# Kernel tuning notes

Measured on AMD Instinct MI355X. Metric: run time of the kernel, lower is better.

## Reference

```python
import jax, jax.numpy as jnp
import numpy as np

B, T, D, NH, FF, L, NCLS, CELL = 4, 64, 128, 4, 512, 2, 7, 64
DIMS = (600, 342, 300)


def layernorm(x, g, b, eps=1e-5):
    m = jnp.mean(x, -1, keepdims=True)
    v = jnp.mean((x - m) ** 2, -1, keepdims=True)
    return (x - m) / jnp.sqrt(v + eps) * g + b


def mha(x, Wqkv, bqkv, Wo, bo):
    N, S, Dm = x.shape
    hd = Dm // NH
    q, k, v = jnp.split(x @ Wqkv + bqkv, 3, axis=-1)
    q = q.reshape(N, S, NH, hd).transpose(0, 2, 1, 3) / jnp.float32(hd) ** 0.5
    k = k.reshape(N, S, NH, hd).transpose(0, 2, 1, 3)
    v = v.reshape(N, S, NH, hd).transpose(0, 2, 1, 3)
    att = jax.nn.softmax(jnp.einsum('nhqd,nhkd->nhqk', q, k), axis=-1)
    o = jnp.einsum('nhqk,nhkd->nhqd', att, v).transpose(0, 2, 1, 3).reshape(N, S, Dm)
    return o @ Wo + bo


def _l2norm(x):
    return x / jnp.maximum(jnp.linalg.norm(x, axis=-1, keepdims=True), 1e-12)


def _model(x_text, x_vis, x_aud, Wp_text, bp_text, Wp_vis, bp_vis, Wp_aud, bp_aud,
           lang1, lang2, Wl1, bl1, Wl2, bl2, phase_text, phase_vis, phase_aud,
           t_Wqkv, t_bqkv, t_Wo, t_bo, t_g1, t_b1, t_W1, t_bf1, t_W2, t_bf2, t_g2, t_b2,
           meas_r, meas_i, fc_W1, fc_b1, fc_W2, fc_b2):
    b, t = x_text.shape[0], x_text.shape[1]
    # modality projections + ReLU
    reps = [jax.nn.relu(x @ W + bb) for x, W, bb in
            ((x_text, Wp_text, bp_text), (x_vis, Wp_vis, bp_vis), (x_aud, Wp_aud, bp_aud))]
    l1 = jnp.broadcast_to(lang1, (b, t, lang1.shape[-1]))
    l2 = jnp.broadcast_to(lang2, (b, t, lang2.shape[-1]))
    lrep1 = jax.nn.relu(l1 @ Wl1 + bl1)
    lrep2 = jax.nn.relu(l2 @ Wl2 + bl2)
    amps = [_l2norm(r) for r in reps]
    lamp1, lamp2 = _l2norm(lrep1), _l2norm(lrep2)
    # phase embedding: smask is all-ones so index is always 0 -> single learned phase vector
    phases = [jnp.broadcast_to(p, (b, t, D)) for p in (phase_text, phase_vis, phase_aud)]
    cmul = lambda ph, a: (a * jnp.cos(ph), a * jnp.sin(ph))
    pure = [cmul(ph, a) for ph, a in zip(phases, amps)]
    ls1 = cmul(phases[0], lamp1)
    ls2 = cmul(phases[0], lamp2)
    # Hadamard gate analog on (real, imag)
    s2 = jnp.float32(2.0) ** -0.5
    h1 = ((ls1[0] + ls1[1]) * s2, (ls1[0] - ls1[1]) * s2)
    h2 = ((ls2[0] + ls2[1]) * s2, (ls2[0] - ls2[1]) * s2)
    # CNOT-style entanglement: complex elementwise product, renormalized to a pure state
    er = h1[0] * h2[0] - h1[1] * h2[1]
    ei = h1[0] * h2[1] + h1[1] * h2[0]
    en = jnp.maximum(jnp.sqrt(jnp.sum(er * er + ei * ei, -1, keepdims=True)), 1e-12)
    ent = (er / en, ei / en)

    def outer(st):  # rho = v v^dagger, v = r + i*im
        r, i = st
        rr = jnp.einsum('btd,bte->btde', r, r) + jnp.einsum('btd,bte->btde', i, i)
        ri = jnp.einsum('btd,bte->btde', i, r) - jnp.einsum('btd,bte->btde', r, i)
        return rr, ri

    mats = [outer(s) for s in pure] + [outer(ent)]
    w = jnp.concatenate([jnp.linalg.norm(r, axis=-1, keepdims=True)
                         for r in reps + [lrep1]], -1)
    w = jax.nn.softmax(w, -1)  # [B,T,4]
    rho_r = sum(w[..., m:m + 1, None] * mats[m][0] for m in range(4))
    rho_i = sum(w[..., m:m + 1, None] * mats[m][1] for m in range(4))
    # seq blocks: same block applied independently per timestep to real and imag parts
    # -> vectorize the Python loop over T (and the real/imag pair) into one batch dim
    x = jnp.concatenate([rho_r, rho_i], 0).reshape(2 * b * t, D, D)
    for l in range(L):
        x = layernorm(x + mha(x, t_Wqkv[l], t_bqkv[l], t_Wo[l], t_bo[l]), t_g1[l], t_b1[l])
        x = layernorm(x + (jax.nn.relu(x @ t_W1[l] + t_bf1[l]) @ t_W2[l] + t_bf2[l]),
                      t_g2[l], t_b2[l])
    x = x.reshape(2, b, t, D, D)
    rho_r, rho_i = x[0], x[1]
    # quantum measurement: p_k = Re(v_k^dagger rho v_k), v_k normalized complex vectors
    mn = jnp.maximum(jnp.sqrt(jnp.sum(meas_r ** 2 + meas_i ** 2, -1, keepdims=True)), 1e-12)
    vr, vi = meas_r / mn, meas_i / mn  # [K=D, D]
    ar = jnp.einsum('btde,ke->btkd', rho_r, vr) - jnp.einsum('btde,ke->btkd', rho_i, vi)
    ai = jnp.einsum('btde,ke->btkd', rho_r, vi) + jnp.einsum('btde,ke->btkd', rho_i, vr)
    probs = jnp.einsum('kd,btkd->btk', vr, ar) + jnp.einsum('kd,btkd->btk', vi, ai)
    logits = jax.nn.relu(probs @ fc_W1 + fc_b1) @ fc_W2 + fc_b2
    return jax.nn.log_softmax(logits, -1)  # [B,T,NCLS]


def setup_inputs():
    key = jax.random.key(0)
    ks = iter(jax.random.split(key, 32))
    rn = lambda shape, s=0.05: jax.random.normal(next(ks), shape, dtype=jnp.float32) * s
    z = lambda shape: jnp.zeros(shape, jnp.float32)
    o = lambda shape: jnp.ones(shape, jnp.float32)
    return dict(
        x_text=rn((B, T, DIMS[0]), 1.0), x_vis=rn((B, T, DIMS[1]), 1.0), x_aud=rn((B, T, DIMS[2]), 1.0),
        Wp_text=rn((DIMS[0], D)), bp_text=z((D,)),
        Wp_vis=rn((DIMS[1], D)), bp_vis=z((D,)),
        Wp_aud=rn((DIMS[2], D)), bp_aud=z((D,)),
        lang1=rn((1, 1, DIMS[2]), 1.0), lang2=rn((1, 1, DIMS[2]), 1.0),
        Wl1=rn((DIMS[2], D)), bl1=z((D,)), Wl2=rn((DIMS[2], D)), bl2=z((D,)),
        phase_text=rn((D,), 1.0), phase_vis=rn((D,), 1.0), phase_aud=rn((D,), 1.0),
        t_Wqkv=rn((L, D, 3 * D)), t_bqkv=z((L, 3 * D)),
        t_Wo=rn((L, D, D)), t_bo=z((L, D)),
        t_g1=o((L, D)), t_b1=z((L, D)),
        t_W1=rn((L, D, FF)), t_bf1=z((L, FF)),
        t_W2=rn((L, FF, D)), t_bf2=z((L, D)),
        t_g2=o((L, D)), t_b2=z((L, D)),
        meas_r=rn((D, D), 1.0), meas_i=rn((D, D), 1.0),
        fc_W1=rn((D, CELL)), fc_b1=z((CELL,)), fc_W2=rn((CELL, NCLS)), fc_b2=z((NCLS,)),
    )


def reference(x_text, x_vis, x_aud, Wp_text, bp_text, Wp_vis, bp_vis, Wp_aud, bp_aud,
              lang1, lang2, Wl1, bl1, Wl2, bl2, phase_text, phase_vis, phase_aud,
              t_Wqkv, t_bqkv, t_Wo, t_bo, t_g1, t_b1, t_W1, t_bf1, t_W2, t_bf2, t_g2, t_b2,
              meas_r, meas_i, fc_W1, fc_b1, fc_W2, fc_b2):
    return _model(x_text, x_vis, x_aud, Wp_text, bp_text, Wp_vis, bp_vis, Wp_aud, bp_aud,
                  lang1, lang2, Wl1, bl1, Wl2, bl2, phase_text, phase_vis, phase_aud,
                  t_Wqkv, t_bqkv, t_Wo, t_bo, t_g1, t_b1, t_W1, t_bf1, t_W2, t_bf2, t_g2, t_b2,
                  meas_r, meas_i, fc_W1, fc_b1, fc_W2, fc_b2)
```

## Files before the change

kernel.cpp:

```cpp
#include <hip/hip_runtime.h>
#include <hip/hip_bf16.h>

typedef __hip_bfloat16 bf16;
typedef short short8 __attribute__((ext_vector_type(8)));
typedef float f32x4 __attribute__((ext_vector_type(4)));

__device__ __forceinline__ float b2f(bf16 v){ return __bfloat162float(v); }

__device__ __forceinline__ short f2bs(float f){
  union { __hip_bfloat16 b; short s; } u; u.b = __float2bfloat16(f); return u.s;
}
__device__ __forceinline__ float bs2f(short s){
  union { short s; __hip_bfloat16 b; } u; u.s = s; return __bfloat162float(u.b);
}

__device__ __forceinline__ float wred_sum(float v){
  #pragma unroll
  for (int o = 32; o > 0; o >>= 1) v += __shfl_xor(v, o, 64);
  return v;
}

__device__ __forceinline__ void gload_lds16(const void* g, void* l){
  __builtin_amdgcn_global_load_lds((const __attribute__((address_space(1))) unsigned*)g,
                                   (__attribute__((address_space(3))) unsigned*)l, 16, 0, 0);
}

__device__ __forceinline__ unsigned swzA(unsigned a){ return a ^ (((a >> 8) & 7u) << 4); }
__device__ __forceinline__ unsigned swzB(unsigned a){ return a ^ (((a >> 7) & 3u) << 4); }

template<int DIMN>
__device__ void modality(const float* x, const float* W, const float* bia, const float* ph,
                         float* PURE, float* RNORM, int m, int bt, float* xs, float* red)
{
  int tid = threadIdx.x;
  for (int i = tid; i < DIMN; i += 128) xs[i] = x[bt*DIMN + i];
  __syncthreads();
  float a0 = 0.f, a1 = 0.f, a2 = 0.f, a3 = 0.f;
  int k = 0;
  for (; k + 4 <= DIMN; k += 4){
    a0 = fmaf(xs[k],   W[(k  )*128 + tid], a0);
    a1 = fmaf(xs[k+1], W[(k+1)*128 + tid], a1);
    a2 = fmaf(xs[k+2], W[(k+2)*128 + tid], a2);
    a3 = fmaf(xs[k+3], W[(k+3)*128 + tid], a3);
  }
  for (; k < DIMN; k++) a0 = fmaf(xs[k], W[k*128 + tid], a0);
  float acc = bia[tid] + ((a0 + a1) + (a2 + a3));
  float rep = fmaxf(acc, 0.f);
  float s = wred_sum(rep*rep);
  int wid = tid >> 6, lane = tid & 63;
  if (lane == 0) red[wid] = s;
  __syncthreads();
  float nrm = sqrtf(red[0] + red[1]);
  float amp = rep / fmaxf(nrm, 1e-12f);
  float p = ph[tid];
  PURE[bt*768 + m*128 + tid]       = amp * cosf(p);
  PURE[bt*768 + (3+m)*128 + tid]   = amp * sinf(p);
  if (tid == 0) RNORM[bt*4 + m] = nrm;
}

__global__ void prep_kernel(
    const float* __restrict__ Wqkv, const float* __restrict__ Wo,
    const float* __restrict__ W1, const float* __restrict__ W2,
    short* __restrict__ WqkvT, short* __restrict__ WoT,
    short* __restrict__ W1T, short* __restrict__ W2T,
    const float* xt, const float* xv, const float* xa,
    const float* Wpt, const float* bpt, const float* Wpv, const float* bpv,
    const float* Wpa, const float* bpa,
    const float* pht, const float* phv, const float* pha,
    float* PURE, float* RNORM,
    const float* l1, const float* l2,
    const float* Wl1, const float* bl1, const float* Wl2, const float* bl2,
    float* LANGB,
    const float* mr, const float* mi, float* VMEAS, short* VMEASB)
{
  __shared__ float xs[600];
  __shared__ float xs2a[300];
  __shared__ float red[4];
  int b = blockIdx.x, tid = threadIdx.x;

  if (b < 384){
    int l = b / 192, bb = b - l*192;
    const float* in; short* out; int K, N, boff;
    bool isW2 = false;
    if (bb < 48)      { in = Wqkv; out = WqkvT; K = 128; N = 384; boff = bb; }
    else if (bb < 64) { in = Wo;   out = WoT;   K = 128; N = 128; boff = bb - 48; }
    else if (bb < 128){ in = W1;   out = W1T;   K = 128; N = 512; boff = bb - 64; }
    else              { in = W2;   out = W2T;   K = 512; N = 128; boff = bb - 128; isW2 = true; }
    int base = l * K * N;
    int i0 = boff * 1024;
    #pragma unroll
    for (int t = 0; t < 8; t++){
      int i = i0 + t*128 + tid;
      if (i < K*N){
        int nn = i / K, kk = i - nn*K;
        int oi = isW2 ? ((kk >> 5)*4096 + nn*32 + (kk & 31)) : i;
        out[base + oi] = f2bs(in[base + kk*N + nn]);
      }
    }
    return;
  }
  if (b < 1152){
    int idx = b - 384;
    int bt = idx & 255, m = idx >> 8;
    if (m == 0)      modality<600>(xt, Wpt, bpt, pht, PURE, RNORM, 0, bt, xs, red);
    else if (m == 1) modality<342>(xv, Wpv, bpv, phv, PURE, RNORM, 1, bt, xs, red);
    else             modality<300>(xa, Wpa, bpa, pha, PURE, RNORM, 2, bt, xs, red);
    return;
  }
  if (b >= 1153){
    int k = b - 1153;
    float a = mr[k*128 + tid], bb2 = mi[k*128 + tid];
    float ws = wred_sum(a*a + bb2*bb2);
    int wid = tid >> 6, lane = tid & 63;
    if (lane == 0) red[wid] = ws;
    __syncthreads();
    float inv = 1.f / fmaxf(sqrtf(red[0] + red[1]), 1e-12f);
    float vr = a * inv, vi = bb2 * inv;
    int i = k*128 + tid;
    VMEAS[i]          = vr;
    VMEAS[16384 + i]  = vi;
    VMEASB[i]         = f2bs(vr);
    VMEASB[16384 + i] = f2bs(vi);
    VMEASB[32768 + i] = f2bs(-vi);
    return;
  }
  for (int i = tid; i < 300; i += 128){ xs[i] = l1[i]; xs2a[i] = l2[i]; }
  __syncthreads();
  float p10=0,p11=0,p12=0,p13=0, p20=0,p21=0,p22=0,p23=0;
  for (int k = 0; k < 300; k += 4){
    p10 = fmaf(xs[k],    Wl1[(k  )*128+tid], p10);
    p11 = fmaf(xs[k+1],  Wl1[(k+1)*128+tid], p11);
    p12 = fmaf(xs[k+2],  Wl1[(k+2)*128+tid], p12);
    p13 = fmaf(xs[k+3],  Wl1[(k+3)*128+tid], p13);
    p20 = fmaf(xs2a[k],  Wl2[(k  )*128+tid], p20);
    p21 = fmaf(xs2a[k+1],Wl2[(k+1)*128+tid], p21);
    p22 = fmaf(xs2a[k+2],Wl2[(k+2)*128+tid], p22);
    p23 = fmaf(xs2a[k+3],Wl2[(k+3)*128+tid], p23);
  }
  float a1 = bl1[tid] + ((p10+p11)+(p12+p13));
  float a2 = bl2[tid] + ((p20+p21)+(p22+p23));
  a1 = fmaxf(a1, 0.f); a2 = fmaxf(a2, 0.f);
  int wid = tid >> 6, lane = tid & 63;
  float s1 = wred_sum(a1*a1), s2 = wred_sum(a2*a2);
  if (lane == 0){ red[wid] = s1; red[2+wid] = s2; }
  __syncthreads();
  float n1 = sqrtf(red[0] + red[1]);
  float n2 = sqrtf(red[2] + red[3]);
  float lamp1 = a1 / fmaxf(n1, 1e-12f);
  float lamp2 = a2 / fmaxf(n2, 1e-12f);
  float ph = pht[tid];
  float c = cosf(ph), s = sinf(ph);
  const float s2c = 0.70710678118654752f;
  float h1r = (lamp1*c + lamp1*s)*s2c, h1i = (lamp1*c - lamp1*s)*s2c;
  float h2r = (lamp2*c + lamp2*s)*s2c, h2i = (lamp2*c - lamp2*s)*s2c;
  float er = h1r*h2r - h1i*h2i;
  float ei = h1r*h2i + h1i*h2r;
  __syncthreads();
  float se = wred_sum(er*er + ei*ei);
  if (lane == 0) red[wid] = se;
  __syncthreads();
  float en = fmaxf(sqrtf(red[0] + red[1]), 1e-12f);
  LANGB[tid]       = er / en;
  LANGB[128 + tid] = ei / en;
  if (tid == 0) LANGB[256] = n1;
}

__global__ __launch_bounds__(256) void rho_kernel(const float* PURE, const float* RNORM,
                                                  const float* LANGB, short* Xb)
{
  __shared__ float rv[4][128], iv[4][128], wsm[4];
  int bt = blockIdx.x >> 1, half = blockIdx.x & 1;
  int tid = threadIdx.x;
  for (int i = tid; i < 1024; i += 256){
    int d = i & 127;
    if (i < 768){ int m = i >> 7; float v = PURE[bt*768 + i];
                  if (m < 3) rv[m][d] = v; else iv[m-3][d] = v; }
    else if (i < 896) rv[3][d] = LANGB[d];
    else              iv[3][d] = LANGB[128 + d];
  }
  if (tid == 0){
    float n0 = RNORM[bt*4+0], n1 = RNORM[bt*4+1], n2 = RNORM[bt*4+2], n3 = LANGB[256];
    float mx = fmaxf(fmaxf(n0, n1), fmaxf(n2, n3));
    float e0 = __expf(n0-mx), e1 = __expf(n1-mx), e2 = __expf(n2-mx), e3 = __expf(n3-mx);
    float inv = 1.f / (e0+e1+e2+e3);
    wsm[0]=e0*inv; wsm[1]=e1*inv; wsm[2]=e2*inv; wsm[3]=e3*inv;
  }
  __syncthreads();
  float w0 = wsm[0], w1 = wsm[1], w2 = wsm[2], w3 = wsm[3];
  int lo = half*8192, hi = lo + 8192;
  for (int idx = lo + tid; idx < hi; idx += 256){
    int d = idx >> 7, e = idx & 127;
    float rr = 0.f, ri = 0.f;
    {
      float rd=rv[0][d], re=rv[0][e], id=iv[0][d], ie=iv[0][e];
      rr = fmaf(w0, rd*re + id*ie, rr); ri = fmaf(w0, id*re - rd*ie, ri);
    }{
      float rd=rv[1][d], re=rv[1][e], id=iv[1][d], ie=iv[1][e];
      rr = fmaf(w1, rd*re + id*ie, rr); ri = fmaf(w1, id*re - rd*ie, ri);
    }{
      float rd=rv[2][d], re=rv[2][e], id=iv[2][d], ie=iv[2][e];
      rr = fmaf(w2, rd*re + id*ie, rr); ri = fmaf(w2, id*re - rd*ie, ri);
    }{
      float rd=rv[3][d], re=rv[3][e], id=iv[3][d], ie=iv[3][e];
      rr = fmaf(w3, rd*re + id*ie, rr); ri = fmaf(w3, id*re - rd*ie, ri);
    }
    Xb[(size_t)bt*16384 + idx]        = f2bs(rr);
    Xb[(size_t)(256+bt)*16384 + idx]  = f2bs(ri);
  }
}

__global__ __launch_bounds__(256) void attn_kernel(const short* __restrict__ Xb,
    const short* __restrict__ WqkvT, const float* __restrict__ bqkv,
    bf16* __restrict__ ATTO)
{
  __shared__ __align__(16) char lds_raw[57344];
  short* Vt = (short*)(lds_raw);
  short* Qs = (short*)(lds_raw + 8704);
  short* Ks = (short*)(lds_raw + 18944);
  short* Ps = (short*)(lds_raw + 8704);

  const int n = blockIdx.x, h = blockIdx.y;
  const int tid = threadIdx.x;
  const int wid = tid >> 6, lane = tid & 63;
  const int l15 = lane & 15, quad = lane >> 4;
  const int wb = __builtin_amdgcn_readfirstlane(wid);
  const short* xn = Xb + (size_t)n*16384;
  const char* Wbase = (const char*)WqkvT;

  #pragma unroll
  for (int j = 0; j < 8; j++){
    unsigned L = (unsigned)(j*4096 + wb*1024 + lane*16);
    gload_lds16((const char*)xn + swzA(L), lds_raw + (j*4096 + wb*1024));
  }
  #pragma unroll
  for (int j = 0; j < 6; j++){
    int seg = wb*6 + j;
    int slab = seg >> 3;
    unsigned off = (unsigned)((seg & 7)*1024);
    unsigned gbase = (unsigned)((slab*128 + h*32)*256);
    gload_lds16(Wbase + gbase + swzA(off + (unsigned)(lane*16)),
                lds_raw + 32768 + seg*1024);
  }
  __syncthreads();

  f32x4 acc[2][6];
  #pragma unroll
  for (int mi = 0; mi < 2; mi++)
    #pragma unroll
    for (int nt = 0; nt < 6; nt++){
      f32x4 z = {0.f, 0.f, 0.f, 0.f}; acc[mi][nt] = z;
    }

  #pragma unroll
  for (int ks = 0; ks < 4; ks++){
    short8 afr[2];
    #pragma unroll
    for (int mi = 0; mi < 2; mi++){
      int row = (wid*2 + mi)*16 + l15;
      unsigned a = (unsigned)(row*256 + ks*64 + quad*16);
      afr[mi] = *(const short8*)(lds_raw + swzA(a));
    }
    #pragma unroll
    for (int nt = 0; nt < 6; nt++){
      int slab = nt >> 1;
      int col = (nt & 1)*16 + l15;
      unsigned a = (unsigned)(col*256 + ks*64 + quad*16);
      short8 bfr = *(const short8*)(lds_raw + 32768 + slab*8192 + swzA(a));
      #pragma unroll
      for (int mi = 0; mi < 2; mi++)
        acc[mi][nt] = __builtin_amdgcn_mfma_f32_16x16x32_bf16(afr[mi], bfr, acc[mi][nt], 0, 0, 0);
    }
  }
  __syncthreads();

  #pragma unroll
  for (int nt = 0; nt < 6; nt++){
    int sec = nt >> 1;
    int cl = (nt & 1)*16 + l15;
    float bias = bqkv[sec*128 + h*32 + cl];
    #pragma unroll
    for (int mi = 0; mi < 2; mi++){
      int rowb = (wid*2 + mi)*16 + quad*4;
      #pragma unroll
      for (int r = 0; r < 4; r++){
        float v = acc[mi][nt][r] + bias;
        int row = rowb + r;
        if (sec == 0)      Qs[row*40 + cl] = f2bs(v * 0.17677669529663687f);
        else if (sec == 1) Ks[row*40 + cl] = f2bs(v);
        else               Vt[cl*136 + row] = f2bs(v);
      }
    }
  }
  __syncthreads();

  f32x4 s[2][8];
  {
    short8 qf[2];
    #pragma unroll
    for (int mi = 0; mi < 2; mi++){
      int row = (wid*2 + mi)*16 + l15;
      qf[mi] = *(const short8*)(Qs + row*40 + quad*8);
    }
    #pragma unroll
    for (int nt = 0; nt < 8; nt++){
      int kr = nt*16 + l15;
      short8 kf = *(const short8*)(Ks + kr*40 + quad*8);
      #pragma unroll
      for (int mi = 0; mi < 2; mi++){
        f32x4 z = {0.f, 0.f, 0.f, 0.f};
        s[mi][nt] = __builtin_amdgcn_mfma_f32_16x16x32_bf16(qf[mi], kf, z, 0, 0, 0);
      }
    }
  }

  #pragma unroll
  for (int mi = 0; mi < 2; mi++){
    #pragma unroll
    for (int r = 0; r < 4; r++){
      float m = -1e30f;
      #pragma unroll
      for (int nt = 0; nt < 8; nt++) m = fmaxf(m, s[mi][nt][r]);
      #pragma unroll
      for (int o = 1; o < 16; o <<= 1) m = fmaxf(m, __shfl_xor(m, o, 64));
      float sum = 0.f;
      #pragma unroll
      for (int nt = 0; nt < 8; nt++){
        float p = __expf(s[mi][nt][r] - m);
        s[mi][nt][r] = p; sum += p;
      }
      #pragma unroll
      for (int o = 1; o < 16; o <<= 1) sum += __shfl_xor(sum, o, 64);
      float inv = 1.f / sum;
      #pragma unroll
      for (int nt = 0; nt < 8; nt++) s[mi][nt][r] *= inv;
    }
  }
  __syncthreads();

  #pragma unroll
  for (int mi = 0; mi < 2; mi++){
    int rowb = (wid*2 + mi)*16 + quad*4;
    #pragma unroll
    for (int nt = 0; nt < 8; nt++){
      int col = nt*16 + l15;
      #pragma unroll
      for (int r = 0; r < 4; r++)
        Ps[(rowb + r)*136 + col] = f2bs(s[mi][nt][r]);
    }
  }
  __syncthreads();

  f32x4 o_[2][2];
  #pragma unroll
  for (int mi = 0; mi < 2; mi++)
    #pragma unroll
    for (int n2 = 0; n2 < 2; n2++){
      f32x4 z = {0.f, 0.f, 0.f, 0.f}; o_[mi][n2] = z;
    }
  #pragma unroll
  for (int ks = 0; ks < 4; ks++){
    short8 pf[2];
    #pragma unroll
    for (int mi = 0; mi < 2; mi++){
      int row = (wid*2 + mi)*16 + l15;
      pf[mi] = *(const short8*)(Ps + row*136 + ks*32 + quad*8);
    }
    #pragma unroll
    for (int n2 = 0; n2 < 2; n2++){
      short8 vf = *(const short8*)(Vt + (n2*16 + l15)*136 + ks*32 + quad*8);
      #pragma unroll
      for (int mi = 0; mi < 2; mi++)
        o_[mi][n2] = __builtin_amdgcn_mfma_f32_16x16x32_bf16(pf[mi], vf, o_[mi][n2], 0, 0, 0);
    }
  }
  bf16* on = ATTO + (size_t)n*16384;
  #pragma unroll
  for (int mi = 0; mi < 2; mi++){
    int rowb = (wid*2 + mi)*16 + quad*4;
    #pragma unroll
    for (int n2 = 0; n2 < 2; n2++){
      int col = h*32 + n2*16 + l15;
      #pragma unroll
      for (int r = 0; r < 4; r++)
        on[(rowb + r)*128 + col] = __float2bfloat16(o_[mi][n2][r]);
    }
  }
}

__global__ __launch_bounds__(256, 2) void proj_ffn_kernel(const bf16* __restrict__ SRC,
    short* __restrict__ Xb, const short* __restrict__ WoT,
    const float* __restrict__ bo, const float* __restrict__ g1v,
    const float* __restrict__ bb1,
    const short* __restrict__ W1T, const float* __restrict__ bf1,
    const short* __restrict__ W2C, const float* __restrict__ bf2,
    const float* __restrict__ g2v, const float* __restrict__ bb2)
{
  __shared__ __align__(16) char lds_raw[65536];
  const int n = blockIdx.x, tid = threadIdx.x;
  const int wid = tid >> 6, lane = tid & 63;
  const int l15 = lane & 15, quad = lane >> 4;
  const int wb = __builtin_amdgcn_readfirstlane(wid);
  const short* an = (const short*)SRC + (size_t)n*16384;
  short* xn = Xb + (size_t)n*16384;
  char* XsB = lds_raw + 32768;
  short* Hs = (short*)(lds_raw + 32768);

  short8 af[2][4];
  #pragma unroll
  for (int mi = 0; mi < 2; mi++)
    #pragma unroll
    for (int ks = 0; ks < 4; ks++){
      int row = wid*32 + mi*16 + l15;
      af[mi][ks] = *(const short8*)(an + row*128 + ks*32 + quad*8);
    }
  #pragma unroll
  for (int j = 0; j < 8; j++){
    unsigned L = (unsigned)(j*4096 + wb*1024 + lane*16);
    gload_lds16((const char*)WoT + swzA(L), lds_raw + (j*4096 + wb*1024));
    gload_lds16((const char*)xn  + swzA(L), XsB + (j*4096 + wb*1024));
  }
  float bov[8], g1a[8], b1a[8];
  #pragma unroll
  for (int nt = 0; nt < 8; nt++){
    int col = nt*16 + l15;
    bov[nt] = bo[col]; g1a[nt] = g1v[col]; b1a[nt] = bb1[col];
  }
  __syncthreads();

  f32x4 Y[2][8];
  #pragma unroll
  for (int mi = 0; mi < 2; mi++)
    #pragma unroll
    for (int nt = 0; nt < 8; nt++){ f32x4 z = {0.f,0.f,0.f,0.f}; Y[mi][nt] = z; }
  #pragma unroll
  for (int ks = 0; ks < 4; ks++){
    #pragma unroll
    for (int nt = 0; nt < 8; nt++){
      unsigned a = (unsigned)((nt*16 + l15)*256 + ks*64 + quad*16);
      short8 bh = *(const short8*)(lds_raw + swzA(a));
      #pragma unroll
      for (int mi = 0; mi < 2; mi++)
        Y[mi][nt] = __builtin_amdgcn_mfma_f32_16x16x32_bf16(af[mi][ks], bh, Y[mi][nt], 0, 0, 0);
    }
  }
  __syncthreads();

  #pragma unroll
  for (int j = 0; j < 2; j++){
    unsigned L = (unsigned)(j*4096 + wb*1024 + lane*16);
    gload_lds16((const char*)W1T + swzA(L), lds_raw + (j*4096 + wb*1024));
    gload_lds16((const char*)W2C + swzB(L), lds_raw + (8192 + j*4096 + wb*1024));
  }

  unsigned yv1p[2][4][4];
  #pragma unroll
  for (int mi = 0; mi < 2; mi++){
    #pragma unroll
    for (int r = 0; r < 4; r++){
      int row = wid*32 + mi*16 + quad*4 + r;
      float yv[8]; float S = 0.f, Q = 0.f;
      #pragma unroll
      for (int nt = 0; nt < 8; nt++){
        int col = nt*16 + l15;
        float res = bs2f(*(const short*)(XsB + swzA((unsigned)(row*256 + col*2))));
        float y = Y[mi][nt][r] + bov[nt] + res;
        yv[nt] = y; S += y; Q += y*y;
      }
      #pragma unroll
      for (int o = 1; o < 16; o <<= 1){ S += __shfl_xor(S, o, 64); Q += __shfl_xor(Q, o, 64); }
      float m = S * (1.f/128.f);
      float var = Q * (1.f/128.f) - m*m;
      float inv = rsqrtf(var + 1e-5f);
      #pragma unroll
      for (int nt = 0; nt < 8; nt++){
        int col = nt*16 + l15;
        short ob = f2bs((yv[nt] - m) * inv * g1a[nt] + b1a[nt]);
        *(short*)(XsB + swzA((unsigned)(row*256 + col*2))) = ob;
        unsigned u = (unsigned)(unsigned short)ob;
        if ((nt & 1) == 0) yv1p[mi][r][nt>>1] = u;
        else               yv1p[mi][r][nt>>1] |= (u << 16);
      }
    }
  }

  short8 af2[2][4];
  #pragma unroll
  for (int mi = 0; mi < 2; mi++)
    #pragma unroll
    for (int ks = 0; ks < 4; ks++){
      int row = wid*32 + mi*16 + l15;
      unsigned a = (unsigned)(row*256 + ks*64 + quad*16);
      af2[mi][ks] = *(const short8*)(XsB + swzA(a));
    }
  __syncthreads();

  f32x4 Y2[2][8];
  #pragma unroll
  for (int mi = 0; mi < 2; mi++)
    #pragma unroll
    for (int nt = 0; nt < 8; nt++){ f32x4 z = {0.f,0.f,0.f,0.f}; Y2[mi][nt] = z; }

  for (int c = 0; c < 16; c++){
    const int cb = c & 1;
    if (c < 15){
      const int nb = cb ^ 1;
      #pragma unroll
      for (int j = 0; j < 2; j++){
        unsigned L = (unsigned)(j*4096 + wb*1024 + lane*16);
        gload_lds16((const char*)W1T + (unsigned)((c+1)*8192) + swzA(L),
                    lds_raw + (nb*16384 + j*4096 + wb*1024));
        gload_lds16((const char*)W2C + (unsigned)((c+1)*8192) + swzB(L),
                    lds_raw + (nb*16384 + 8192 + j*4096 + wb*1024));
      }
    }
    const char* bW1 = lds_raw + cb*16384;
    const char* bW2 = lds_raw + cb*16384 + 8192;

    f32x4 Hc[2][2];
    #pragma unroll
    for (int mi = 0; mi < 2; mi++)
      #pragma unroll
      for (int nt2 = 0; nt2 < 2; nt2++){ f32x4 z = {0.f,0.f,0.f,0.f}; Hc[mi][nt2] = z; }
    #pragma unroll
    for (int ks = 0; ks < 4; ks++){
      #pragma unroll
      for (int nt2 = 0; nt2 < 2; nt2++){
        unsigned a = (unsigned)((nt2*16 + l15)*256 + ks*64 + quad*16);
        short8 bh = *(const short8*)(bW1 + swzA(a));
        #pragma unroll
        for (int mi = 0; mi < 2; mi++)
          Hc[mi][nt2] = __builtin_amdgcn_mfma_f32_16x16x32_bf16(af2[mi][ks], bh, Hc[mi][nt2], 0, 0, 0);
      }
    }
    float b1v0 = bf1[c*32 + l15];
    float b1v1 = bf1[c*32 + 16 + l15];
    #pragma unroll
    for (int nt2 = 0; nt2 < 2; nt2++){
      int col = nt2*16 + l15;
      float b1v = nt2 ? b1v1 : b1v0;
      #pragma unroll
      for (int mi = 0; mi < 2; mi++){
        int rowb = wid*32 + mi*16 + quad*4;
        #pragma unroll
        for (int r = 0; r < 4; r++)
          Hs[(rowb + r)*40 + col] = f2bs(fmaxf(Hc[mi][nt2][r] + b1v, 0.f));
      }
    }
    short8 ph[2];
    #pragma unroll
    for (int mi = 0; mi < 2; mi++){
      int row = wid*32 + mi*16 + l15;
      ph[mi] = *(const short8*)(Hs + row*40 + quad*8);
    }
    #pragma unroll
    for (int nt = 0; nt < 8; nt++){
      unsigned a = (unsigned)((nt*16 + l15)*64 + quad*16);
      short8 bh = *(const short8*)(bW2 + swzB(a));
      #pragma unroll
      for (int mi = 0; mi < 2; mi++)
        Y2[mi][nt] = __builtin_amdgcn_mfma_f32_16x16x32_bf16(ph[mi], bh, Y2[mi][nt], 0, 0, 0);
    }
    if (c < 15) __syncthreads();
  }

  {
    float b2v[8], gv[8], bbv[8];
    #pragma unroll
    for (int nt = 0; nt < 8; nt++){
      int col = nt*16 + l15;
      b2v[nt] = bf2[col]; gv[nt] = g2v[col]; bbv[nt] = bb2[col];
    }
    #pragma unroll
    for (int mi = 0; mi < 2; mi++){
      #pragma unroll
      for (int r = 0; r < 4; r++){
        int row = wid*32 + mi*16 + quad*4 + r;
        float yv[8]; float S = 0.f, Q = 0.f;
        #pragma unroll
        for (int nt = 0; nt < 8; nt++){
          unsigned u = yv1p[mi][r][nt>>1];
          short rs = (short)((nt & 1) ? (u >> 16) : (u & 0xffffu));
          float y = Y2[mi][nt][r] + b2v[nt] + bs2f(rs);
          yv[nt] = y; S += y; Q += y*y;
        }
        #pragma unroll
        for (int o = 1; o < 16; o <<= 1){ S += __shfl_xor(S, o, 64); Q += __shfl_xor(Q, o, 64); }
        float m = S * (1.f/128.f);
        float var = Q * (1.f/128.f) - m*m;
        float inv = rsqrtf(var + 1e-5f);
        #pragma unroll
        for (int nt = 0; nt < 8; nt++){
          int col = nt*16 + l15;
          xn[row*128 + col] = f2bs((yv[nt] - m) * inv * gv[nt] + bbv[nt]);
        }
      }
    }
  }
}

__global__ __launch_bounds__(256) void probs_kernel(const short* __restrict__ Xb,
    const float* __restrict__ VMEAS, const short* __restrict__ VMEASB,
    float* __restrict__ PROBS)
{
  __shared__ float sp[128];
  const int bt = blockIdx.x, z = blockIdx.y, tid = threadIdx.x;
  const int wid = tid >> 6, lane = tid & 63;
  const int l15 = lane & 15, quad = lane >> 4;
  const short* R = Xb + (size_t)bt*16384;
  const short* I = Xb + (size_t)(256+bt)*16384;
  const short* vrB  = VMEASB;
  const short* viB  = VMEASB + 16384;
  const short* nviB = VMEASB + 32768;

  if (tid < 128) sp[tid] = 0.f;
  __syncthreads();

  const int drow = z*64 + wid*16 + l15;
  short8 aR[4], aI[4];
  #pragma unroll
  for (int ks = 0; ks < 4; ks++){
    aR[ks] = *(const short8*)(R + drow*128 + ks*32 + quad*8);
    aI[ks] = *(const short8*)(I + drow*128 + ks*32 + quad*8);
  }

  float p[8];
  #pragma unroll
  for (int nt = 0; nt < 8; nt++) p[nt] = 0.f;
  const int db = z*64 + wid*16 + quad*4;

  {
    f32x4 Ar[8];
    #pragma unroll
    for (int nt = 0; nt < 8; nt++){ f32x4 zz = {0.f,0.f,0.f,0.f}; Ar[nt] = zz; }
    #pragma unroll
    for (int ks = 0; ks < 4; ks++){
      #pragma unroll
      for (int nt = 0; nt < 8; nt++){
        int coln = nt*16 + l15;
        short8 b1 = *(const short8*)(vrB  + coln*128 + ks*32 + quad*8);
        short8 b2 = *(const short8*)(nviB + coln*128 + ks*32 + quad*8);
        Ar[nt] = __builtin_amdgcn_mfma_f32_16x16x32_bf16(aR[ks], b1, Ar[nt], 0, 0, 0);
        Ar[nt] = __builtin_amdgcn_mfma_f32_16x16x32_bf16(aI[ks], b2, Ar[nt], 0, 0, 0);
      }
    }
    #pragma unroll
    for (int nt = 0; nt < 8; nt++){
      int k = nt*16 + l15;
      #pragma unroll
      for (int r = 0; r < 4; r++)
        p[nt] = fmaf(VMEAS[k*128 + db + r], Ar[nt][r], p[nt]);
    }
  }
  {
    f32x4 Ai[8];
    #pragma unroll
    for (int nt = 0; nt < 8; nt++){ f32x4 zz = {0.f,0.f,0.f,0.f}; Ai[nt] = zz; }
    #pragma unroll
    for (int ks = 0; ks < 4; ks++){
      #pragma unroll
      for (int nt = 0; nt < 8; nt++){
        int coln = nt*16 + l15;
        short8 b1 = *(const short8*)(viB + coln*128 + ks*32 + quad*8);
        short8 b2 = *(const short8*)(vrB + coln*128 + ks*32 + quad*8);
        Ai[nt] = __builtin_amdgcn_mfma_f32_16x16x32_bf16(aR[ks], b1, Ai[nt], 0, 0, 0);
        Ai[nt] = __builtin_amdgcn_mfma_f32_16x16x32_bf16(aI[ks], b2, Ai[nt], 0, 0, 0);
      }
    }
    #pragma unroll
    for (int nt = 0; nt < 8; nt++){
      int k = nt*16 + l15;
      #pragma unroll
      for (int r = 0; r < 4; r++)
        p[nt] = fmaf(VMEAS[16384 + k*128 + db + r], Ai[nt][r], p[nt]);
    }
  }

  #pragma unroll
  for (int nt = 0; nt < 8; nt++){
    float v = p[nt];
    v += __shfl_xor(v, 16, 64);
    v += __shfl_xor(v, 32, 64);
    if (quad == 0) atomicAdd(&sp[nt*16 + l15], v);
  }
  __syncthreads();
  if (tid < 128) PROBS[(size_t)(z*256 + bt)*128 + tid] = sp[tid];
}

__global__ void head_kernel(const float* PROBS, const float* W1, const float* b1,
                            const float* W2, const float* b2, float* out)
{
  __shared__ float h[64];
  __shared__ float lg[7];
  __shared__ float mred[2];
  int bt = blockIdx.x, tid = threadIdx.x;
  float a0 = b1[tid], a1 = 0.f, a2 = 0.f, a3 = 0.f;
  for (int d = 0; d < 128; d += 4){
    float p0 = PROBS[bt*128 + d  ] + PROBS[(256+bt)*128 + d  ];
    float p1 = PROBS[bt*128 + d+1] + PROBS[(256+bt)*128 + d+1];
    float p2 = PROBS[bt*128 + d+2] + PROBS[(256+bt)*128 + d+2];
    float p3 = PROBS[bt*128 + d+3] + PROBS[(256+bt)*128 + d+3];
    a0 = fmaf(p0, W1[(d  )*64 + tid], a0);
    a1 = fmaf(p1, W1[(d+1)*64 + tid], a1);
    a2 = fmaf(p2, W1[(d+2)*64 + tid], a2);
    a3 = fmaf(p3, W1[(d+3)*64 + tid], a3);
  }
  h[tid] = fmaxf((a0 + a1) + (a2 + a3), 0.f);
  __syncthreads();
  if (tid < 7){
    float a = b2[tid];
    for (int j = 0; j < 64; j++) a = fmaf(h[j], W2[j*7 + tid], a);
    lg[tid] = a;
  }
  __syncthreads();
  if (tid == 0){
    float M = -1e30f;
    for (int c = 0; c < 7; c++) M = fmaxf(M, lg[c]);
    float S = 0.f;
    for (int c = 0; c < 7; c++) S += __expf(lg[c] - M);
    mred[0] = M; mred[1] = logf(S);
  }
  __syncthreads();
  if (tid < 7) out[bt*7 + tid] = lg[tid] - mred[0] - mred[1];
}

extern "C" void kernel_launch(void* const* d_in, const int* in_sizes, int n_in,
                              void* d_out, int out_size, void* d_ws, size_t ws_size,
                              hipStream_t stream)
{
  (void)in_sizes; (void)n_in; (void)out_size; (void)ws_size;
  const float* xt   = (const float*)d_in[0];
  const float* xv   = (const float*)d_in[1];
  const float* xa   = (const float*)d_in[2];
  const float* Wpt  = (const float*)d_in[3];
  const float* bpt  = (const float*)d_in[4];
  const float* Wpv  = (const float*)d_in[5];
  const float* bpv  = (const float*)d_in[6];
  const float* Wpa  = (const float*)d_in[7];
  const float* bpa  = (const float*)d_in[8];
  const float* l1   = (const float*)d_in[9];
  const float* l2   = (const float*)d_in[10];
  const float* Wl1  = (const float*)d_in[11];
  const float* bl1  = (const float*)d_in[12];
  const float* Wl2  = (const float*)d_in[13];
  const float* bl2  = (const float*)d_in[14];
  const float* pht  = (const float*)d_in[15];
  const float* phv  = (const float*)d_in[16];
  const float* pha  = (const float*)d_in[17];
  const float* Wqkv = (const float*)d_in[18];
  const float* bqkv = (const float*)d_in[19];
  const float* Wo   = (const float*)d_in[20];
  const float* bo   = (const float*)d_in[21];
  const float* g1   = (const float*)d_in[22];
  const float* b1   = (const float*)d_in[23];
  const float* W1   = (const float*)d_in[24];
  const float* bf1  = (const float*)d_in[25];
  const float* W2   = (const float*)d_in[26];
  const float* bf2  = (const float*)d_in[27];
  const float* g2   = (const float*)d_in[28];
  const float* b2   = (const float*)d_in[29];
  const float* mr   = (const float*)d_in[30];
  const float* mi   = (const float*)d_in[31];
  const float* fcW1 = (const float*)d_in[32];
  const float* fcb1 = (const float*)d_in[33];
  const float* fcW2 = (const float*)d_in[34];
  const float* fcb2 = (const float*)d_in[35];
  float* out = (float*)d_out;

  char* wsb = (char*)d_ws;
  short* Xb     = (short*)(wsb);
  bf16*  ATTO   = (bf16*) (wsb + 16777216);
  float* PURE   = (float*)(wsb + 33554432);
  float* RNORM  = (float*)(wsb + 34340864);
  float* LANGB  = (float*)(wsb + 34344960);
  float* VMEAS  = (float*)(wsb + 34347008);
  float* PROBS  = (float*)(wsb + 34478080);
  short* WqkvT  = (short*)(wsb + 34740224);
  short* WoT    = (short*)(wsb + 34936832);
  short* W1T    = (short*)(wsb + 35002368);
  short* W2T    = (short*)(wsb + 35264512);
  short* VMEASB = (short*)(wsb + 35526656);

  prep_kernel<<<1281, 128, 0, stream>>>(Wqkv, Wo, W1, W2, WqkvT, WoT, W1T, W2T,
                                        xt, xv, xa, Wpt, bpt, Wpv, bpv, Wpa, bpa,
                                        pht, phv, pha, PURE, RNORM,
                                        l1, l2, Wl1, bl1, Wl2, bl2, LANGB,
                                        mr, mi, VMEAS, VMEASB);

  rho_kernel<<<512, 256, 0, stream>>>(PURE, RNORM, LANGB, Xb);

  for (int l = 0; l < 2; l++){
    attn_kernel<<<dim3(512, 4), 256, 0, stream>>>(Xb, WqkvT + (size_t)l*49152,
                                                  bqkv + (size_t)l*384, ATTO);
    proj_ffn_kernel<<<512, 256, 0, stream>>>(ATTO, Xb,
                                             WoT + (size_t)l*16384,
                                             bo + (size_t)l*128, g1 + (size_t)l*128,
                                             b1 + (size_t)l*128,
                                             W1T + (size_t)l*65536, bf1 + (size_t)l*512,
                                             W2T + (size_t)l*65536, bf2 + (size_t)l*128,
                                             g2 + (size_t)l*128, b2 + (size_t)l*128);
  }

  probs_kernel<<<dim3(256, 2), 256, 0, stream>>>(Xb, VMEAS, VMEASB, PROBS);
  head_kernel<<<256, 64, 0, stream>>>(PROBS, fcW1, fcb1, fcW2, fcb2, out);
}
```

Measured before the change: 318.1 us.

## Load attention A fragments to registers and double-buffer measurement weights through LDS

In the attention kernel, the X activation fragments are now read directly from global memory into registers instead of being staged through LDS, which lowers the LDS footprint so more blocks can fit per CU. In the probs kernel, the measurement weight matrices are double-buffered in LDS with async global-to-LDS loads per column tile, replacing the direct global fragment reads. Each tile is reduced right away with vectorized VMEAS loads, which lowers register pressure. The cost is a block barrier on every iteration, and the direct global A loads bypass the swizzled LDS layout.

```diff
diff --git a/kernel.cpp b/kernel.cpp
--- a/kernel.cpp
+++ b/kernel.cpp
@@ -213,7 +213,7 @@
     const short* __restrict__ WqkvT, const float* __restrict__ bqkv,
     bf16* __restrict__ ATTO)
 {
-  __shared__ __align__(16) char lds_raw[57344];
+  __shared__ __align__(16) char lds_raw[43520];
   short* Vt = (short*)(lds_raw);
   short* Qs = (short*)(lds_raw + 8704);
   short* Ks = (short*)(lds_raw + 18944);
@@ -227,11 +227,14 @@
   const short* xn = Xb + (size_t)n*16384;
   const char* Wbase = (const char*)WqkvT;
 
-  #pragma unroll
-  for (int j = 0; j < 8; j++){
-    unsigned L = (unsigned)(j*4096 + wb*1024 + lane*16);
-    gload_lds16((const char*)xn + swzA(L), lds_raw + (j*4096 + wb*1024));
-  }
+  short8 afr[2][4];
+  #pragma unroll
+  for (int mi = 0; mi < 2; mi++)
+    #pragma unroll
+    for (int ks = 0; ks < 4; ks++){
+      int row = (wid*2 + mi)*16 + l15;
+      afr[mi][ks] = *(const short8*)(xn + row*128 + ks*32 + quad*8);
+    }
   #pragma unroll
   for (int j = 0; j < 6; j++){
     int seg = wb*6 + j;
@@ -239,7 +242,7 @@
     unsigned off = (unsigned)((seg & 7)*1024);
     unsigned gbase = (unsigned)((slab*128 + h*32)*256);
     gload_lds16(Wbase + gbase + swzA(off + (unsigned)(lane*16)),
-                lds_raw + 32768 + seg*1024);
+                lds_raw + seg*1024);
   }
   __syncthreads();
 
@@ -253,22 +256,15 @@
 
   #pragma unroll
   for (int ks = 0; ks < 4; ks++){
-    short8 afr[2];
-    #pragma unroll
-    for (int mi = 0; mi < 2; mi++){
-      int row = (wid*2 + mi)*16 + l15;
-      unsigned a = (unsigned)(row*256 + ks*64 + quad*16);
-      afr[mi] = *(const short8*)(lds_raw + swzA(a));
-    }
     #pragma unroll
     for (int nt = 0; nt < 6; nt++){
       int slab = nt >> 1;
       int col = (nt & 1)*16 + l15;
       unsigned a = (unsigned)(col*256 + ks*64 + quad*16);
-      short8 bfr = *(const short8*)(lds_raw + 32768 + slab*8192 + swzA(a));
+      short8 bfr = *(const short8*)(lds_raw + slab*8192 + swzA(a));
       #pragma unroll
       for (int mi = 0; mi < 2; mi++)
-        acc[mi][nt] = __builtin_amdgcn_mfma_f32_16x16x32_bf16(afr[mi], bfr, acc[mi][nt], 0, 0, 0);
+        acc[mi][nt] = __builtin_amdgcn_mfma_f32_16x16x32_bf16(afr[mi][ks], bfr, acc[mi][nt], 0, 0, 0);
     }
   }
   __syncthreads();
@@ -602,18 +598,16 @@
     const float* __restrict__ VMEAS, const short* __restrict__ VMEASB,
     float* __restrict__ PROBS)
 {
+  __shared__ __align__(16) char lds_raw[24576];
   __shared__ float sp[128];
   const int bt = blockIdx.x, z = blockIdx.y, tid = threadIdx.x;
   const int wid = tid >> 6, lane = tid & 63;
   const int l15 = lane & 15, quad = lane >> 4;
+  const int wb = __builtin_amdgcn_readfirstlane(wid);
   const short* R = Xb + (size_t)bt*16384;
   const short* I = Xb + (size_t)(256+bt)*16384;
-  const short* vrB  = VMEASB;
-  const short* viB  = VMEASB + 16384;
-  const short* nviB = VMEASB + 32768;
 
   if (tid < 128) sp[tid] = 0.f;
-  __syncthreads();
 
   const int drow = z*64 + wid*16 + l15;
   short8 aR[4], aI[4];
@@ -623,66 +617,58 @@
     aI[ks] = *(const short8*)(I + drow*128 + ks*32 + quad*8);
   }
 
-  float p[8];
-  #pragma unroll
-  for (int nt = 0; nt < 8; nt++) p[nt] = 0.f;
+  #define STAGE_NT(nt_, buf_)                                                  \
+    { _Pragma("unroll")                                                        \
+      for (int j = 0; j < 3; j++){                                             \
+        int seg = wb*3 + j;                                         \
+        int s = seg >> 2;                                       \
+        unsigned off = (unsigned)((seg & 3)*1024);                             \
+        gload_lds16((const char*)VMEASB + s*32768 + (nt_)*4096 +               \
+                      swzA(off + (unsigned)(lane*16)),                         \
+                    lds_raw + (buf_)*12288 + s*4096 + (int)off);               \
+      } }
+
+  STAGE_NT(0, 0)
+  __syncthreads();
+
   const int db = z*64 + wid*16 + quad*4;
 
-  {
-    f32x4 Ar[8];
-    #pragma unroll
-    for (int nt = 0; nt < 8; nt++){ f32x4 zz = {0.f,0.f,0.f,0.f}; Ar[nt] = zz; }
+  for (int nt = 0; nt < 8; nt++){
+    const int cb = nt & 1;
+    if (nt < 7) STAGE_NT(nt+1, cb^1)
+
+    const char* bvr = lds_raw + cb*12288;
+    const char* bvi = bvr + 4096;
+    const char* bnv = bvr + 8192;
+
+    f32x4 Ar = {0.f,0.f,0.f,0.f}, Ai = {0.f,0.f,0.f,0.f};
     #pragma unroll
     for (int ks = 0; ks < 4; ks++){
-      #pragma unroll
-      for (int nt = 0; nt < 8; nt++){
-        int coln = nt*16 + l15;
-        short8 b1 = *(const short8*)(vrB  + coln*128 + ks*32 + quad*8);
-        short8 b2 = *(const short8*)(nviB + coln*128 + ks*32 + quad*8);
-        Ar[nt] = __builtin_amdgcn_mfma_f32_16x16x32_bf16(aR[ks], b1, Ar[nt], 0, 0, 0);
-        Ar[nt] = __builtin_amdgcn_mfma_f32_16x16x32_bf16(aI[ks], b2, Ar[nt], 0, 0, 0);
-      }
-    }
-    #pragma unroll
-    for (int nt = 0; nt < 8; nt++){
-      int k = nt*16 + l15;
-      #pragma unroll
-      for (int r = 0; r < 4; r++)
-        p[nt] = fmaf(VMEAS[k*128 + db + r], Ar[nt][r], p[nt]);
-    }
-  }
-  {
-    f32x4 Ai[8];
-    #pragma unroll
-    for (int nt = 0; nt < 8; nt++){ f32x4 zz = {0.f,0.f,0.f,0.f}; Ai[nt] = zz; }
-    #pragma unroll
-    for (int ks = 0; ks < 4; ks++){
-      #pragma unroll
-      for (int nt = 0; nt < 8; nt++){
-        int coln = nt*16 + l15;
-        short8 b1 = *(const short8*)(viB + coln*128 + ks*32 + quad*8);
-        short8 b2 = *(const short8*)(vrB + coln*128 + ks*32 + quad*8);
-        Ai[nt] = __builtin_amdgcn_mfma_f32_16x16x32_bf16(aR[ks], b1, Ai[nt], 0, 0, 0);
-        Ai[nt] = __builtin_amdgcn_mfma_f32_16x16x32_bf16(aI[ks], b2, Ai[nt], 0, 0, 0);
-      }
-    }
-    #pragma unroll
-    for (int nt = 0; nt < 8; nt++){
-      int k = nt*16 + l15;
-      #pragma unroll
-      for (int r = 0; r < 4; r++)
-        p[nt] = fmaf(VMEAS[16384 + k*128 + db + r], Ai[nt][r], p[nt]);
-    }
-  }
-
-  #pragma unroll
-  for (int nt = 0; nt < 8; nt++){
-    float v = p[nt];
-    v += __shfl_xor(v, 16, 64);
-    v += __shfl_xor(v, 32, 64);
-    if (quad == 0) atomicAdd(&sp[nt*16 + l15], v);
-  }
-  __syncthreads();
+      unsigned a = swzA((unsigned)(l15*256 + ks*64 + quad*16));
+      short8 b_vr = *(const short8*)(bvr + a);
+      short8 b_vi = *(const short8*)(bvi + a);
+      short8 b_nv = *(const short8*)(bnv + a);
+      Ar = __builtin_amdgcn_mfma_f32_16x16x32_bf16(aR[ks], b_vr, Ar, 0, 0, 0);
+      Ar = __builtin_amdgcn_mfma_f32_16x16x32_bf16(aI[ks], b_nv, Ar, 0, 0, 0);
+      Ai = __builtin_amdgcn_mfma_f32_16x16x32_bf16(aR[ks], b_vi, Ai, 0, 0, 0);
+      Ai = __builtin_amdgcn_mfma_f32_16x16x32_bf16(aI[ks], b_vr, Ai, 0, 0, 0);
+    }
+
+    int k = nt*16 + l15;
+    f32x4 vR = *(const f32x4*)(VMEAS + k*128 + db);
+    f32x4 vI = *(const f32x4*)(VMEAS + 16384 + k*128 + db);
+    float pv = 0.f;
+    #pragma unroll
+    for (int r = 0; r < 4; r++) pv += vR[r]*Ar[r] + vI[r]*Ai[r];
+
+    pv += __shfl_xor(pv, 16, 64);
+    pv += __shfl_xor(pv, 32, 64);
+    if (quad == 0) atomicAdd(&sp[nt*16 + l15], pv);
+
+    __syncthreads();
+  }
+  #undef STAGE_NT
+
   if (tid < 128) PROBS[(size_t)(z*256 + bt)*128 + tid] = sp[tid];
 }
 
```

Result: faster. 290.6 us (-8.7%).
